# Kernel tuning notes

Measured on AMD Instinct MI355X. Metric: run time of the kernel, lower is better.

The kernel has to match this reference:

```python
import jax, jax.numpy as jnp
import numpy as np

H, W, N, G = 256, 256, 4096, 4
CHOL_BOUND = np.array([0.5, 0.0, 0.5], np.float32)

def _haar_highpass(x):
    # level-1 haar wavedec -> waverec with approx coeffs zeroed
    n = len(x) - (len(x) % 2)
    pairs = x[:n].reshape(-1, 2)
    d = (pairs[:, 0] - pairs[:, 1]) / np.sqrt(2.0)
    rec = np.zeros(len(x), np.float32)
    rec[0:n:2] = d / np.sqrt(2.0)
    rec[1:n:2] = -d / np.sqrt(2.0)
    return rec

def setup_inputs():
    rng = np.random.RandomState(0)
    xyz = rng.randn(N, 2).astype(np.float32)
    chol = (rng.randn(N, 3) * 0.1).astype(np.float32)
    feats = rng.rand(N, 3).astype(np.float32)
    opac = np.ones((N, 1), np.float32)
    hf = np.stack([_haar_highpass(xyz[:, i]) for i in range(2)], 1)
    mag = np.linalg.norm(hf, axis=1)
    thr = np.quantile(mag, 0.75)  # deterministic 75/25 split -> Nl=3072, Nh=1024
    high = mag > thr
    low = ~high
    nh = int(high.sum())
    gabor_freqs = (0.1 + 0.01 * rng.randn(nh * G, 2)).astype(np.float32)
    gabor_weights = (0.01 + 0.001 * rng.randn(nh * G, 1)).astype(np.float32)
    return {
        'low_mu': jnp.asarray(xyz[low]), 'high_mu': jnp.asarray(xyz[high]),
        'low_chol': jnp.asarray(chol[low]), 'high_chol': jnp.asarray(chol[high]),
        'low_feat': jnp.asarray(feats[low]), 'high_feat': jnp.asarray(feats[high]),
        'low_opac': jnp.asarray(opac[low]), 'high_opac': jnp.asarray(opac[high]),
        'gabor_freqs': jnp.asarray(gabor_freqs),
        'gabor_weights': jnp.asarray(gabor_weights),
    }

def _project(mu, chol):
    # project_gaussians_2d: tanh(mu) in [-1,1] -> pixel coords; Sigma = L L^T, conic = Sigma^-1
    m = jnp.tanh(mu)
    xy = jnp.stack([(m[:, 0] + 1.0) * 0.5 * W, (m[:, 1] + 1.0) * 0.5 * H], -1)
    ch = chol + jnp.asarray(CHOL_BOUND)
    l1, l2, l3 = ch[:, 0], ch[:, 1], ch[:, 2]
    sxx, sxy, syy = l1 * l1, l1 * l2, l2 * l2 + l3 * l3
    det = sxx * syy - sxy * sxy
    conic = jnp.stack([syy / det, -sxy / det, sxx / det], -1)  # (A, B, C)
    return xy, conic

def _pad(a, m):
    return jnp.concatenate([a, jnp.zeros((m - a.shape[0],) + a.shape[1:], a.dtype)], 0)

def _sigma(xyc, cc, xs, ys):
    dx = xs[None, :] - xyc[:, 0:1]  # [C,W]
    dy = ys[None, :] - xyc[:, 1:2]  # [C,H]
    return (0.5 * cc[:, 0, None, None] * dx[:, None, :] ** 2
            + cc[:, 1, None, None] * dy[:, :, None] * dx[:, None, :]
            + 0.5 * cc[:, 2, None, None] * dy[:, :, None] ** 2)  # [C,H,W]

def _raster_gauss(xy, conic, colors, opac, chunk=256):
    # rasterize_gaussians_sum: out(p) = sum_i opac_i * exp(-sigma_i(p)) * color_i
    xs = jnp.arange(W, dtype=jnp.float32) + 0.5
    ys = jnp.arange(H, dtype=jnp.float32) + 0.5
    m = ((xy.shape[0] + chunk - 1) // chunk) * chunk
    parts = tuple(_pad(a, m).reshape(-1, chunk, a.shape[1]) for a in (xy, conic, colors, opac))
    def body(acc, sl):
        xyc, cc, col, op = sl
        wgt = op[:, 0, None, None] * jnp.exp(-_sigma(xyc, cc, xs, ys))
        return acc + jnp.einsum('chw,ck->hwk', wgt, col), None
    acc, _ = jax.lax.scan(body, jnp.zeros((H, W, 3), jnp.float32), parts)
    return acc

def _raster_gabor(xy, conic, colors, opac, freqs, weights, chunk=64):
    # rasterize_gabor_sum: gaussian envelope modulated by a weighted sum of G cosine carriers
    xs = jnp.arange(W, dtype=jnp.float32) + 0.5
    ys = jnp.arange(H, dtype=jnp.float32) + 0.5
    n = xy.shape[0]
    fx = freqs[:, 0].reshape(n, G)
    fy = freqs[:, 1].reshape(n, G)
    wg = weights[:, 0].reshape(n, G)
    m = ((n + chunk - 1) // chunk) * chunk
    parts = tuple(_pad(a, m).reshape(-1, chunk, a.shape[1]) for a in (xy, conic, colors, opac, fx, fy, wg))
    def body(acc, sl):
        xyc, cc, col, op, fxc, fyc, wc = sl
        dx = xs[None, :] - xyc[:, 0:1]
        dy = ys[None, :] - xyc[:, 1:2]
        phase = (fxc[:, :, None, None] * dx[:, None, None, :]
                 + fyc[:, :, None, None] * dy[:, None, :, None])  # [C,G,H,W]
        mod = jnp.sum(wc[:, :, None, None] * jnp.cos(phase), axis=1)  # [C,H,W]
        wgt = op[:, 0, None, None] * jnp.exp(-_sigma(xyc, cc, xs, ys)) * mod
        return acc + jnp.einsum('chw,ck->hwk', wgt, col), None
    acc, _ = jax.lax.scan(body, jnp.zeros((H, W, 3), jnp.float32), parts)
    return acc

def reference(low_mu, high_mu, low_chol, high_chol, low_feat, high_feat,
              low_opac, high_opac, gabor_freqs, gabor_weights):
    xy_l, con_l = _project(low_mu, low_chol)
    xy_h, con_h = _project(high_mu, high_chol)
    out_low = _raster_gauss(xy_l, con_l, low_feat, low_opac)
    out_high = _raster_gabor(xy_h, con_h, high_feat, high_opac, gabor_freqs, gabor_weights)
    img = jnp.clip(out_low + out_high, 0.0, 1.0)  # [H,W,3]
    return img.transpose(2, 0, 1)[None]  # [1,3,H,W]
```

## Files before the change

### kernel.cpp

```cpp
#include <hip/hip_runtime.h>

#define IMG_W 256
#define IMG_H 256
#define GG 4
#define CUT 15.0f

__global__ __launch_bounds__(256) void project_kernel(
    const float* __restrict__ low_mu,   const float* __restrict__ low_chol,
    const float* __restrict__ low_feat, const float* __restrict__ low_opac,
    const float* __restrict__ high_mu,  const float* __restrict__ high_chol,
    const float* __restrict__ high_feat,const float* __restrict__ high_opac,
    const float* __restrict__ gfreq,    const float* __restrict__ gweight,
    int nl, int nh,
    float* __restrict__ plow, float* __restrict__ phigh)
{
    int i = blockIdx.x * blockDim.x + threadIdx.x;
    if (i >= nl + nh) return;
    bool islow = (i < nl);
    int k = islow ? i : (i - nl);
    const float* mu   = islow ? low_mu   : high_mu;
    const float* chol = islow ? low_chol : high_chol;
    const float* feat = islow ? low_feat : high_feat;
    const float* opac = islow ? low_opac : high_opac;

    float m0 = tanhf(mu[2*k]);
    float m1 = tanhf(mu[2*k+1]);
    float cx = (m0 + 1.0f) * 0.5f * (float)IMG_W;
    float cy = (m1 + 1.0f) * 0.5f * (float)IMG_H;

    float l1 = chol[3*k]     + 0.5f;
    float l2 = chol[3*k + 1];
    float l3 = chol[3*k + 2] + 0.5f;
    float sxx = l1*l1, sxy = l1*l2, syy = l2*l2 + l3*l3;
    float det = sxx*syy - sxy*sxy;
    float inv = 1.0f / det;
    float q0 = syy*inv, q1 = -sxy*inv, q2 = sxx*inv;

    float ht = 0.5f*(q0 + q2);
    float hd = 0.5f*(q0 - q2);
    float lam = ht - sqrtf(hd*hd + q1*q1);
    lam = fmaxf(lam, 1e-6f);
    float rad = sqrtf(2.0f * CUT / lam) + 1.0f;

    float op = opac[k];
    float pr = feat[3*k]*op, pg = feat[3*k+1]*op, pb = feat[3*k+2]*op;

    if (islow) {
        float* p = plow + (size_t)k * 12;
        p[0]=cx; p[1]=cy; p[2]=0.5f*q0; p[3]=q1; p[4]=0.5f*q2; p[5]=rad;
        p[6]=pr; p[7]=pg; p[8]=pb; p[9]=0.f; p[10]=0.f; p[11]=0.f;
    } else {
        float* p = phigh + (size_t)k * 24;
        p[0]=cx; p[1]=cy; p[2]=0.5f*q0; p[3]=q1; p[4]=0.5f*q2; p[5]=rad;
        p[6]=pr; p[7]=pg; p[8]=pb; p[9]=0.f; p[10]=0.f; p[11]=0.f;
        #pragma unroll
        for (int g = 0; g < GG; ++g) {
            p[12+g] = gfreq[(k*GG + g)*2];
            p[16+g] = gfreq[(k*GG + g)*2 + 1];
            p[20+g] = gweight[k*GG + g];
        }
    }
}

__global__ __launch_bounds__(256) void raster_kernel(
    const float* __restrict__ plow, int nl,
    const float* __restrict__ phigh, int nh,
    float* __restrict__ out)
{
    __shared__ int s_cnt;
    __shared__ int s_list[4096];

    const int tid = threadIdx.x;
    const int bx = blockIdx.x & 15, by = blockIdx.x >> 4;
    const float tx0 = bx*16 + 0.5f, ty0 = by*16 + 0.5f;
    const float tx1 = tx0 + 15.0f,  ty1 = ty0 + 15.0f;
    const int lx = tid & 15, ly = tid >> 4;
    const float px = bx*16 + lx + 0.5f;
    const float py = by*16 + ly + 0.5f;

    float accr = 0.f, accg = 0.f, accb = 0.f;

    if (tid == 0) s_cnt = 0;
    __syncthreads();
    for (int i = tid; i < nl; i += 256) {
        const float* p = plow + (size_t)i * 12;
        float cx = p[0], cy = p[1], rad = p[5];
        if (cx + rad >= tx0 && cx - rad <= tx1 &&
            cy + rad >= ty0 && cy - rad <= ty1) {
            int slot = atomicAdd(&s_cnt, 1);
            s_list[slot] = i;
        }
    }
    __syncthreads();
    int cnt = s_cnt;
    for (int j = 0; j < cnt; ++j) {
        int idx = __builtin_amdgcn_readfirstlane(s_list[j]);
        const float* p = plow + (size_t)idx * 12;
        float dx = px - p[0], dy = py - p[1];
        float s  = (p[2]*dx + p[3]*dy)*dx + p[4]*dy*dy;
        float e  = __expf(-s);
        accr = fmaf(e, p[6], accr);
        accg = fmaf(e, p[7], accg);
        accb = fmaf(e, p[8], accb);
    }
    __syncthreads();

    if (tid == 0) s_cnt = 0;
    __syncthreads();
    for (int i = tid; i < nh; i += 256) {
        const float* p = phigh + (size_t)i * 24;
        float cx = p[0], cy = p[1], rad = p[5];
        if (cx + rad >= tx0 && cx - rad <= tx1 &&
            cy + rad >= ty0 && cy - rad <= ty1) {
            int slot = atomicAdd(&s_cnt, 1);
            s_list[slot] = i;
        }
    }
    __syncthreads();
    cnt = s_cnt;
    for (int j = 0; j < cnt; ++j) {
        int idx = __builtin_amdgcn_readfirstlane(s_list[j]);
        const float* p = phigh + (size_t)idx * 24;
        float dx = px - p[0], dy = py - p[1];
        float s  = (p[2]*dx + p[3]*dy)*dx + p[4]*dy*dy;
        float e  = __expf(-s);
        float mod = 0.f;
        #pragma unroll
        for (int g = 0; g < GG; ++g) {
            float ph = p[12+g]*dx + p[16+g]*dy;
            mod = fmaf(p[20+g], __cosf(ph), mod);
        }
        float e2 = e * mod;
        accr = fmaf(e2, p[6], accr);
        accg = fmaf(e2, p[7], accg);
        accb = fmaf(e2, p[8], accb);
    }

    int x = bx*16 + lx, y = by*16 + ly;
    int pix = y*IMG_W + x;
    out[pix]                 = fminf(fmaxf(accr, 0.f), 1.f);
    out[IMG_H*IMG_W + pix]   = fminf(fmaxf(accg, 0.f), 1.f);
    out[2*IMG_H*IMG_W + pix] = fminf(fmaxf(accb, 0.f), 1.f);
}

extern "C" void kernel_launch(void* const* d_in, const int* in_sizes, int n_in,
                              void* d_out, int out_size, void* d_ws, size_t ws_size,
                              hipStream_t stream)
{
    const float* low_mu    = (const float*)d_in[0];
    const float* high_mu   = (const float*)d_in[1];
    const float* low_chol  = (const float*)d_in[2];
    const float* high_chol = (const float*)d_in[3];
    const float* low_feat  = (const float*)d_in[4];
    const float* high_feat = (const float*)d_in[5];
    const float* low_opac  = (const float*)d_in[6];
    const float* high_opac = (const float*)d_in[7];
    const float* gfreq     = (const float*)d_in[8];
    const float* gweight   = (const float*)d_in[9];

    int nl = in_sizes[0] / 2;
    int nh = in_sizes[1] / 2;

    float* plow  = (float*)d_ws;
    float* phigh = plow + (size_t)nl * 12;
    float* out   = (float*)d_out;

    int n = nl + nh;
    project_kernel<<<(n + 255) / 256, 256, 0, stream>>>(
        low_mu, low_chol, low_feat, low_opac,
        high_mu, high_chol, high_feat, high_opac,
        gfreq, gweight, nl, nh, plow, phigh);

    raster_kernel<<<256, 256, 0, stream>>>(plow, nl, phigh, nh, out);
}
```

Measured before the change: 91.80 us.

## Fuse projection into raster kernel with batched shared-memory culled primitive lists

Drops the separate projection kernel. Each raster block now re-projects every Gaussian in batches of 512, culls them against its tile, and writes the surviving parameters straight into shared memory, so the inner loop reads LDS instead of global memory. The exponent is prescaled by log2e so the loop can use exp2, and Gabor frequencies are prescaled by 1/2π so it can use the hardware cos on a fract'd argument. The cost is redundant projection work in all 256 blocks (tanh, sqrt, divide per Gaussian per block) and more block-wide barriers per batch.

```diff
diff --git a/kernel.cpp b/kernel.cpp
--- a/kernel.cpp
+++ b/kernel.cpp
@@ -4,71 +4,56 @@
 #define IMG_H 256
 #define GG 4
 #define CUT 15.0f
+#define LOG2E  1.44269504088896340736f
+#define INV2PI 0.15915494309189533577f
 
-__global__ __launch_bounds__(256) void project_kernel(
+#define BATCH 512
+#define LSTRIDE 8
+#define HSTRIDE 20
+
+struct Proj { float cx, cy, A, B, C, rad, pr, pg, pb; };
+
+__device__ __forceinline__ Proj project_one(
+    const float* __restrict__ mu,   const float* __restrict__ chol,
+    const float* __restrict__ feat, const float* __restrict__ opac, int k)
+{
+    Proj o;
+    float2 m = ((const float2*)mu)[k];
+    float m0 = tanhf(m.x), m1 = tanhf(m.y);
+    o.cx = (m0 + 1.0f) * (0.5f * (float)IMG_W);
+    o.cy = (m1 + 1.0f) * (0.5f * (float)IMG_H);
+
+    const float* c = chol + 3*(size_t)k;
+    float l1 = c[0] + 0.5f, l2 = c[1], l3 = c[2] + 0.5f;
+    float sxx = l1*l1, sxy = l1*l2, syy = l2*l2 + l3*l3;
+    float det = sxx*syy - sxy*sxy;
+    float inv = 1.0f / det;
+    float q0 = syy*inv, q1 = -sxy*inv, q2 = sxx*inv;
+
+    float ht = 0.5f*(q0+q2), hd = 0.5f*(q0-q2);
+    float lam = fmaxf(ht - sqrtf(hd*hd + q1*q1), 1e-6f);
+    o.rad = sqrtf(2.0f*CUT/lam) + 1.0f;
+
+    o.A = -0.5f*q0*LOG2E;
+    o.B = -q1*LOG2E;
+    o.C = -0.5f*q2*LOG2E;
+
+    float op = opac[k];
+    const float* f = feat + 3*(size_t)k;
+    o.pr = f[0]*op; o.pg = f[1]*op; o.pb = f[2]*op;
+    return o;
+}
+
+__global__ __launch_bounds__(256) void raster_fused(
     const float* __restrict__ low_mu,   const float* __restrict__ low_chol,
     const float* __restrict__ low_feat, const float* __restrict__ low_opac,
     const float* __restrict__ high_mu,  const float* __restrict__ high_chol,
     const float* __restrict__ high_feat,const float* __restrict__ high_opac,
     const float* __restrict__ gfreq,    const float* __restrict__ gweight,
-    int nl, int nh,
-    float* __restrict__ plow, float* __restrict__ phigh)
+    int nl, int nh, float* __restrict__ out)
 {
-    int i = blockIdx.x * blockDim.x + threadIdx.x;
-    if (i >= nl + nh) return;
-    bool islow = (i < nl);
-    int k = islow ? i : (i - nl);
-    const float* mu   = islow ? low_mu   : high_mu;
-    const float* chol = islow ? low_chol : high_chol;
-    const float* feat = islow ? low_feat : high_feat;
-    const float* opac = islow ? low_opac : high_opac;
-
-    float m0 = tanhf(mu[2*k]);
-    float m1 = tanhf(mu[2*k+1]);
-    float cx = (m0 + 1.0f) * 0.5f * (float)IMG_W;
-    float cy = (m1 + 1.0f) * 0.5f * (float)IMG_H;
-
-    float l1 = chol[3*k]     + 0.5f;
-    float l2 = chol[3*k + 1];
-    float l3 = chol[3*k + 2] + 0.5f;
-    float sxx = l1*l1, sxy = l1*l2, syy = l2*l2 + l3*l3;
-    float det = sxx*syy - sxy*sxy;
-    float inv = 1.0f / det;
-    float q0 = syy*inv, q1 = -sxy*inv, q2 = sxx*inv;
-
-    float ht = 0.5f*(q0 + q2);
-    float hd = 0.5f*(q0 - q2);
-    float lam = ht - sqrtf(hd*hd + q1*q1);
-    lam = fmaxf(lam, 1e-6f);
-    float rad = sqrtf(2.0f * CUT / lam) + 1.0f;
-
-    float op = opac[k];
-    float pr = feat[3*k]*op, pg = feat[3*k+1]*op, pb = feat[3*k+2]*op;
-
-    if (islow) {
-        float* p = plow + (size_t)k * 12;
-        p[0]=cx; p[1]=cy; p[2]=0.5f*q0; p[3]=q1; p[4]=0.5f*q2; p[5]=rad;
-        p[6]=pr; p[7]=pg; p[8]=pb; p[9]=0.f; p[10]=0.f; p[11]=0.f;
-    } else {
-        float* p = phigh + (size_t)k * 24;
-        p[0]=cx; p[1]=cy; p[2]=0.5f*q0; p[3]=q1; p[4]=0.5f*q2; p[5]=rad;
-        p[6]=pr; p[7]=pg; p[8]=pb; p[9]=0.f; p[10]=0.f; p[11]=0.f;
-        #pragma unroll
-        for (int g = 0; g < GG; ++g) {
-            p[12+g] = gfreq[(k*GG + g)*2];
-            p[16+g] = gfreq[(k*GG + g)*2 + 1];
-            p[20+g] = gweight[k*GG + g];
-        }
-    }
-}
-
-__global__ __launch_bounds__(256) void raster_kernel(
-    const float* __restrict__ plow, int nl,
-    const float* __restrict__ phigh, int nh,
-    float* __restrict__ out)
-{
-    __shared__ int s_cnt;
-    __shared__ int s_list[4096];
+    __shared__ float s_buf[BATCH * HSTRIDE];
+    __shared__ int   s_cnt[2];
 
     const int tid = threadIdx.x;
     const int bx = blockIdx.x & 15, by = blockIdx.x >> 4;
@@ -80,60 +65,86 @@
 
     float accr = 0.f, accg = 0.f, accb = 0.f;
 
-    if (tid == 0) s_cnt = 0;
-    __syncthreads();
-    for (int i = tid; i < nl; i += 256) {
-        const float* p = plow + (size_t)i * 12;
-        float cx = p[0], cy = p[1], rad = p[5];
-        if (cx + rad >= tx0 && cx - rad <= tx1 &&
-            cy + rad >= ty0 && cy - rad <= ty1) {
-            int slot = atomicAdd(&s_cnt, 1);
-            s_list[slot] = i;
-        }
-    }
-    __syncthreads();
-    int cnt = s_cnt;
-    for (int j = 0; j < cnt; ++j) {
-        int idx = __builtin_amdgcn_readfirstlane(s_list[j]);
-        const float* p = plow + (size_t)idx * 12;
-        float dx = px - p[0], dy = py - p[1];
-        float s  = (p[2]*dx + p[3]*dy)*dx + p[4]*dy*dy;
-        float e  = __expf(-s);
-        accr = fmaf(e, p[6], accr);
-        accg = fmaf(e, p[7], accg);
-        accb = fmaf(e, p[8], accb);
-    }
+    if (tid < 2) s_cnt[tid] = 0;
     __syncthreads();
 
-    if (tid == 0) s_cnt = 0;
-    __syncthreads();
-    for (int i = tid; i < nh; i += 256) {
-        const float* p = phigh + (size_t)i * 24;
-        float cx = p[0], cy = p[1], rad = p[5];
-        if (cx + rad >= tx0 && cx - rad <= tx1 &&
-            cy + rad >= ty0 && cy - rad <= ty1) {
-            int slot = atomicAdd(&s_cnt, 1);
-            s_list[slot] = i;
+    int par = 0;
+
+    for (int base = 0; base < nl; base += BATCH, par ^= 1) {
+        if (tid == 0) s_cnt[par ^ 1] = 0;
+        #pragma unroll
+        for (int u = 0; u < BATCH/256; ++u) {
+            int i = base + u*256 + tid;
+            if (i < nl) {
+                Proj p = project_one(low_mu, low_chol, low_feat, low_opac, i);
+                if (p.cx + p.rad >= tx0 && p.cx - p.rad <= tx1 &&
+                    p.cy + p.rad >= ty0 && p.cy - p.rad <= ty1) {
+                    int slot = atomicAdd(&s_cnt[par], 1);
+                    float4* q = (float4*)(s_buf + slot*LSTRIDE);
+                    q[0] = make_float4(p.cx, p.cy, p.A, p.B);
+                    q[1] = make_float4(p.C,  p.pr, p.pg, p.pb);
+                }
+            }
         }
+        __syncthreads();
+        int cnt = s_cnt[par];
+        for (int j = 0; j < cnt; ++j) {
+            const float4* q = (const float4*)(s_buf + j*LSTRIDE);
+            float4 a = q[0], b = q[1];
+            float dx = px - a.x, dy = py - a.y;
+            float s2 = (a.z*dx + a.w*dy)*dx + b.x*dy*dy;
+            float e  = __builtin_amdgcn_exp2f(s2);
+            accr = fmaf(e, b.y, accr);
+            accg = fmaf(e, b.z, accg);
+            accb = fmaf(e, b.w, accb);
+        }
+        __syncthreads();
     }
-    __syncthreads();
-    cnt = s_cnt;
-    for (int j = 0; j < cnt; ++j) {
-        int idx = __builtin_amdgcn_readfirstlane(s_list[j]);
-        const float* p = phigh + (size_t)idx * 24;
-        float dx = px - p[0], dy = py - p[1];
-        float s  = (p[2]*dx + p[3]*dy)*dx + p[4]*dy*dy;
-        float e  = __expf(-s);
-        float mod = 0.f;
+
+    for (int base = 0; base < nh; base += BATCH, par ^= 1) {
+        if (tid == 0) s_cnt[par ^ 1] = 0;
         #pragma unroll
-        for (int g = 0; g < GG; ++g) {
-            float ph = p[12+g]*dx + p[16+g]*dy;
-            mod = fmaf(p[20+g], __cosf(ph), mod);
+        for (int u = 0; u < BATCH/256; ++u) {
+            int i = base + u*256 + tid;
+            if (i < nh) {
+                Proj p = project_one(high_mu, high_chol, high_feat, high_opac, i);
+                if (p.cx + p.rad >= tx0 && p.cx - p.rad <= tx1 &&
+                    p.cy + p.rad >= ty0 && p.cy - p.rad <= ty1) {
+                    int slot = atomicAdd(&s_cnt[par], 1);
+                    float* q = s_buf + slot*HSTRIDE;
+                    ((float4*)q)[0] = make_float4(p.cx, p.cy, p.A, p.B);
+                    ((float4*)q)[1] = make_float4(p.C,  p.pr, p.pg, p.pb);
+                    #pragma unroll
+                    for (int g = 0; g < GG; ++g) {
+                        float2 f = ((const float2*)gfreq)[i*GG + g];
+                        q[8  + g] = f.x * INV2PI;
+                        q[12 + g] = f.y * INV2PI;
+                        q[16 + g] = gweight[i*GG + g];
+                    }
+                }
+            }
         }
-        float e2 = e * mod;
-        accr = fmaf(e2, p[6], accr);
-        accg = fmaf(e2, p[7], accg);
-        accb = fmaf(e2, p[8], accb);
+        __syncthreads();
+        int cnt = s_cnt[par];
+        for (int j = 0; j < cnt; ++j) {
+            const float* q = s_buf + j*HSTRIDE;
+            float4 a = ((const float4*)q)[0], b = ((const float4*)q)[1];
+            float dx = px - a.x, dy = py - a.y;
+            float s2 = (a.z*dx + a.w*dy)*dx + b.x*dy*dy;
+            float e  = __builtin_amdgcn_exp2f(s2);
+            float mod = 0.f;
+            #pragma unroll
+            for (int g = 0; g < GG; ++g) {
+                float ph = q[8+g]*dx + q[12+g]*dy;
+                float fr = __builtin_amdgcn_fractf(ph);
+                mod = fmaf(q[16+g], __builtin_amdgcn_cosf(fr), mod);
+            }
+            float e2 = e * mod;
+            accr = fmaf(e2, b.y, accr);
+            accg = fmaf(e2, b.z, accg);
+            accb = fmaf(e2, b.w, accb);
+        }
+        __syncthreads();
     }
 
     int x = bx*16 + lx, y = by*16 + ly;
@@ -161,15 +172,10 @@
     int nl = in_sizes[0] / 2;
     int nh = in_sizes[1] / 2;
 
-    float* plow  = (float*)d_ws;
-    float* phigh = plow + (size_t)nl * 12;
-    float* out   = (float*)d_out;
+    (void)d_ws; (void)ws_size;
 
-    int n = nl + nh;
-    project_kernel<<<(n + 255) / 256, 256, 0, stream>>>(
+    raster_fused<<<256, 256, 0, stream>>>(
         low_mu, low_chol, low_feat, low_opac,
         high_mu, high_chol, high_feat, high_opac,
-        gfreq, gweight, nl, nh, plow, phigh);
-
-    raster_kernel<<<256, 256, 0, stream>>>(plow, nl, phigh, nh, out);
+        gfreq, gweight, nl, nh, (float*)d_out);
 }
```

Measured after the change: 92.39 us. No clear change (+0.6%).
